# Performance work log

Measured on AMD Instinct MI355X. Metric: run time of the kernel, lower is better.

## Reference

```python
import jax, jax.numpy as jnp
import numpy as np

K_GAUSS = 7      # gaussian_kernel_size
K_CONV = 5       # base-kernel conv size
SIGMA_MIN = 0.01
SIGMA_MAX = 1.0


def setup_inputs() -> dict:
    key = jax.random.key(0)
    k1, k2, k3 = jax.random.split(key, 3)
    input_data = jax.random.normal(k1, (8, 3, 224, 224), dtype=jnp.float32)
    foa_xy = jax.random.randint(k2, (8, 2), 0, 224)  # (x=row, y=col) fixation per sample
    weight = jax.random.normal(k3, (64, 3, K_CONV, K_CONV), dtype=jnp.float32) * 0.05
    return {"input_data": input_data, "foa_xy": foa_xy, "weight": weight}


def _extract_patches(x, k):
    # torch.nn.functional.unfold with stride=1, dilation=1, padding=k//2
    # x: (b,c,h,w) -> (b,c,k*k,h*w); patch flat index = ki*k + kj (row-major)
    b, c, h, w = x.shape
    p = k // 2
    xp = jnp.pad(x, ((0, 0), (0, 0), (p, p), (p, p)))
    shifts = [xp[:, :, i:i + h, j:j + w] for i in range(k) for j in range(k)]
    return jnp.stack(shifts, axis=2).reshape(b, c, k * k, h * w)


def _gaussian_modulate(x, foa_xy):
    # GaussianFOAConv2d: per-pixel normalized Gaussian kernel, sigma linear in distance from FOA
    b, c, h, w = x.shape
    hw = h * w
    ii, jj = jnp.meshgrid(jnp.arange(h, dtype=jnp.float32),
                          jnp.arange(w, dtype=jnp.float32), indexing='ij')
    xy = jnp.stack([ii, jj], axis=-1).reshape(hw, 2)           # (hw,2): (row, col)
    foa = foa_xy.astype(jnp.float32)                            # (b,2)
    dists = jnp.linalg.norm(xy[None, :, :] - foa[:, None, :], axis=-1)
    dists = dists / np.float32(np.sqrt(h ** 2 + w ** 2))        # (b,hw) in [0,1]
    sigmas = (1.0 - dists) * SIGMA_MIN + dists * SIGMA_MAX      # (b,hw)
    r = jnp.arange(-(K_GAUSS // 2), K_GAUSS // 2 + 1, dtype=jnp.float32)
    d2 = (r[:, None] ** 2 + r[None, :] ** 2).reshape(-1)        # (kk,) row-major, matches patch order
    kern = jnp.exp(-d2[None, :, None] / (2.0 * sigmas[:, None, :] ** 2))  # (b,kk,hw)
    kern = kern / jnp.sum(kern, axis=1, keepdims=True)
    patches = _extract_patches(x, K_GAUSS)                      # (b,c,kk,hw)
    out = jnp.einsum('bckp,bkp->bcp', patches, kern)            # spatial-only kernel -> sum over kk
    return out.reshape(b, c, h, w)


def reference(input_data, foa_xy, weight):
    # 1) Gaussian input modulation driven by FOA distance
    modulated = _gaussian_modulate(input_data, foa_xy)
    # 2) classic convolution with the learnable base kernel (stride 1, 'same' padding, no bias)
    p = K_CONV // 2
    return jax.lax.conv_general_dilated(
        modulated, weight, window_strides=(1, 1), padding=((p, p), (p, p)),
        dimension_numbers=('NCHW', 'OIHW', 'NCHW'))
```

## Files before the change

### kernel.cpp

```cpp
#include <hip/hip_runtime.h>

#define H 224
#define W 224
#define HW (224 * 224)
#define CIN 3
#define OCH 64

#define TS 32
#define MN 36
#define MSTH 40
#define RN 42
#define RST 44

typedef __attribute__((ext_vector_type(8))) short short8;
typedef __attribute__((ext_vector_type(4))) float f32x4;

__device__ __forceinline__ unsigned f2bf_pk(float lo, float hi) {
    unsigned a = __float_as_uint(lo), b = __float_as_uint(hi);
    a = (a + 0x7FFFu + ((a >> 16) & 1u)) >> 16;
    b = (b + 0x7FFFu + ((b >> 16) & 1u)) & 0xFFFF0000u;
    return a | b;
}

__global__ void make_wA(const float* __restrict__ w, uint4* __restrict__ wA) {
    int t = threadIdx.x;
    int lane = t & 63;
    int fi = t >> 6;
    int mt = fi >> 2, S = fi & 3;
    int q = lane >> 4;
    int oc = mt * 16 + (lane & 15);
    float v[8];
#pragma unroll
    for (int j = 0; j < 8; ++j) {
        float x = 0.f;
        if (j < 5) {
            if (S < 3) x = w[oc * 75 + S * 25 + q * 5 + j];
            else if (q < 3) x = w[oc * 75 + q * 25 + 20 + j];
        }
        v[j] = x;
    }
    uint4 r;
    r.x = f2bf_pk(v[0], v[1]);
    r.y = f2bf_pk(v[2], v[3]);
    r.z = f2bf_pk(v[4], v[5]);
    r.w = f2bf_pk(v[6], v[7]);
    wA[fi * 64 + lane] = r;
}

__global__ __launch_bounds__(256, 2) void fused(
    const uint4* __restrict__ wA, const float* __restrict__ in,
    const int* __restrict__ foa, float* __restrict__ out)
{
    __shared__ float  s_raw[CIN][RN][RST];
    __shared__ ushort s_mod[CIN][MN][MSTH];

    int tid = threadIdx.x;
    int lane = tid & 63;
    int tx0 = blockIdx.x * TS, ty0 = blockIdx.y * TS, b = blockIdx.z;

    short8 aw[4][4];
#pragma unroll
    for (int mt = 0; mt < 4; ++mt)
#pragma unroll
        for (int S = 0; S < 4; ++S) {
            union { uint4 u4; short8 s8; } cv;
            cv.u4 = wA[(mt * 4 + S) * 64 + lane];
            aw[mt][S] = cv.s8;
        }

    const float* src = in + (size_t)b * CIN * HW;
    for (int i = tid; i < CIN * RN * RN; i += 256) {
        int ch = i / (RN * RN);
        int rem = i - ch * (RN * RN);
        int rr = rem / RN;
        int cc = rem - rr * RN;
        int gr = ty0 - 5 + rr, gc = tx0 - 5 + cc;
        float v = 0.f;
        if ((unsigned)gr < H && (unsigned)gc < W) v = src[ch * HW + gr * W + gc];
        s_raw[ch][rr][cc] = v;
    }
    __syncthreads();

    float fr = (float)foa[2 * b + 0], fc = (float)foa[2 * b + 1];
    for (int u = tid; u < CIN * MN * 9; u += 256) {
        int ch = u / (MN * 9);
        int rem = u - ch * (MN * 9);
        int rm = rem / 9;
        int qc = rem - rm * 9;
        int cm0 = qc * 4;
        int gr = ty0 - 2 + rm;

        float pw[4][7], inv[4];
#pragma unroll
        for (int o = 0; o < 4; ++o) {
            int gc = tx0 - 2 + cm0 + o;
            float dr = (float)gr - fr, dc = (float)gc - fc;
            float dist = sqrtf(dr * dr + dc * dc) * 3.1567268e-3f;
            float sigma = 0.01f + 0.99f * dist;
            float ae = -0.5f / (sigma * sigma);
            float e1 = __expf(ae);
            float e2 = e1 * e1, e4 = e2 * e2, e9 = e4 * e4 * e1;
            pw[o][0] = e9; pw[o][1] = e4; pw[o][2] = e1; pw[o][3] = 1.f;
            pw[o][4] = e1; pw[o][5] = e4; pw[o][6] = e9;
            float S = 1.f + 2.f * (e1 + e4 + e9);
            inv[o] = 1.f / (S * S);
        }
        float acc[4] = {0.f, 0.f, 0.f, 0.f};
#pragma unroll
        for (int ki = 0; ki < 7; ++ki) {
            const float* rp = &s_raw[ch][rm + ki][cm0];
            float rv[10];
            *(f32x4*)&rv[0] = *(const f32x4*)rp;
            *(f32x4*)&rv[4] = *(const f32x4*)(rp + 4);
            *(float2*)&rv[8] = *(const float2*)(rp + 8);
#pragma unroll
            for (int o = 0; o < 4; ++o) {
                float rs = 0.f;
#pragma unroll
                for (int kj = 0; kj < 7; ++kj) rs += pw[o][kj] * rv[o + kj];
                acc[o] += pw[o][ki] * rs;
            }
        }
        float res[4];
#pragma unroll
        for (int o = 0; o < 4; ++o) {
            int gc = tx0 - 2 + cm0 + o;
            bool ok = ((unsigned)gr < H) && ((unsigned)gc < W);
            res[o] = ok ? acc[o] * inv[o] : 0.f;
        }
        uint2 st;
        st.x = f2bf_pk(res[0], res[1]);
        st.y = f2bf_pk(res[2], res[3]);
        *(uint2*)&s_mod[ch][rm][cm0] = st;
    }
    __syncthreads();

    int wv = tid >> 6;
    int q = lane >> 4, li = lane & 15;

#pragma unroll
    for (int r8 = 0; r8 < 8; ++r8) {
        int ro = wv * 8 + r8;
#pragma unroll
        for (int s = 0; s < 2; ++s) {
            int co = s * 16 + li;
            int cd = co >> 1;
            unsigned sel = (unsigned)(co & 1) * 16u;

            short8 bf[4];
#pragma unroll
            for (int S = 0; S < 4; ++S) {
                int ch = (S < 3) ? S : (q < 3 ? q : 2);
                int rm = (S < 3) ? (ro + q) : (ro + 4);
                const unsigned* p = (const unsigned*)&s_mod[ch][rm][0] + cd;
                unsigned u0 = p[0], u1 = p[1], u2 = p[2];
                union { unsigned u[4]; short8 s8; } cv;
                cv.u[0] = __builtin_amdgcn_alignbit(u1, u0, sel);
                cv.u[1] = __builtin_amdgcn_alignbit(u2, u1, sel);
                cv.u[2] = u2 >> sel;
                cv.u[3] = 0;
                bf[S] = cv.s8;
            }

            f32x4 acc[4];
#pragma unroll
            for (int mt = 0; mt < 4; ++mt) acc[mt] = (f32x4){0.f, 0.f, 0.f, 0.f};
#pragma unroll
            for (int S = 0; S < 4; ++S)
#pragma unroll
                for (int mt = 0; mt < 4; ++mt)
                    acc[mt] = __builtin_amdgcn_mfma_f32_16x16x32_bf16(
                        aw[mt][S], bf[S], acc[mt], 0, 0, 0);

            int px = tx0 + co, py = ty0 + ro;
#pragma unroll
            for (int mt = 0; mt < 4; ++mt) {
#pragma unroll
                for (int r = 0; r < 4; ++r) {
                    int oc = mt * 16 + q * 4 + r;
                    out[(size_t)(b * OCH + oc) * HW + (size_t)py * W + px] = acc[mt][r];
                }
            }
        }
    }
}

extern "C" void kernel_launch(void* const* d_in, const int* in_sizes, int n_in,
                              void* d_out, int out_size, void* d_ws, size_t ws_size,
                              hipStream_t stream) {
    const float* input  = (const float*)d_in[0];
    const int*   foa    = (const int*)d_in[1];
    const float* weight = (const float*)d_in[2];
    float* outp = (float*)d_out;

    uint4* wA = (uint4*)d_ws;

    make_wA<<<1, 1024, 0, stream>>>(weight, wA);

    dim3 grid(W / TS, H / TS, 8);
    fused<<<grid, 256, 0, stream>>>(wA, input, foa, outp);
}
```

Baseline: 126.4 us.

## Give each wave a private halo tile to remove block-wide barriers

Each of the four waves now loads its own 18x42 raw halo and computes its own 12-row modulated strip in a private shared-memory slice, so the two __syncthreads are dropped and waves proceed independently. The goal is to remove barrier stalls and let each wave's load, Gaussian and MFMA phases overlap with those of other waves. In exchange, halo rows are loaded and modulated redundantly across waves (18 rows per 8 output rows instead of 42 per 32), and shared memory grows to about 51 KB, which may limit occupancy. No barrier is needed within a wave because the writes and reads stay inside a single wavefront.

```diff
diff --git a/kernel.cpp b/kernel.cpp
--- a/kernel.cpp
+++ b/kernel.cpp
@@ -7,10 +7,12 @@
 #define OCH 64
 
 #define TS 32
-#define MN 36
-#define MSTH 40
-#define RN 42
-#define RST 44
+#define WRN 18
+#define WRC 42
+#define WRST 44
+#define WMN 12
+#define WMC 36
+#define WMST 40
 
 typedef __attribute__((ext_vector_type(8))) short short8;
 typedef __attribute__((ext_vector_type(4))) float f32x4;
@@ -51,12 +53,15 @@
     const uint4* __restrict__ wA, const float* __restrict__ in,
     const int* __restrict__ foa, float* __restrict__ out)
 {
-    __shared__ float  s_raw[CIN][RN][RST];
-    __shared__ ushort s_mod[CIN][MN][MSTH];
+    __shared__ float  s_raw[4][CIN][WRN][WRST];
+    __shared__ ushort s_mod[4][CIN][WMN][WMST];
 
     int tid = threadIdx.x;
     int lane = tid & 63;
-    int tx0 = blockIdx.x * TS, ty0 = blockIdx.y * TS, b = blockIdx.z;
+    int wv = tid >> 6;
+    int tx0 = blockIdx.x * TS;
+    int ty0 = blockIdx.y * TS + wv * 8;
+    int b = blockIdx.z;
 
     short8 aw[4][4];
 #pragma unroll
@@ -69,22 +74,21 @@
         }
 
     const float* src = in + (size_t)b * CIN * HW;
-    for (int i = tid; i < CIN * RN * RN; i += 256) {
-        int ch = i / (RN * RN);
-        int rem = i - ch * (RN * RN);
-        int rr = rem / RN;
-        int cc = rem - rr * RN;
+    for (int i = lane; i < CIN * WRN * WRC; i += 64) {
+        int ch = i / (WRN * WRC);
+        int rem = i - ch * (WRN * WRC);
+        int rr = rem / WRC;
+        int cc = rem - rr * WRC;
         int gr = ty0 - 5 + rr, gc = tx0 - 5 + cc;
         float v = 0.f;
         if ((unsigned)gr < H && (unsigned)gc < W) v = src[ch * HW + gr * W + gc];
-        s_raw[ch][rr][cc] = v;
-    }
-    __syncthreads();
+        s_raw[wv][ch][rr][cc] = v;
+    }
 
     float fr = (float)foa[2 * b + 0], fc = (float)foa[2 * b + 1];
-    for (int u = tid; u < CIN * MN * 9; u += 256) {
-        int ch = u / (MN * 9);
-        int rem = u - ch * (MN * 9);
+    for (int u = lane; u < CIN * WMN * 9; u += 64) {
+        int ch = u / (WMN * 9);
+        int rem = u - ch * (WMN * 9);
         int rm = rem / 9;
         int qc = rem - rm * 9;
         int cm0 = qc * 4;
@@ -108,7 +112,7 @@
         float acc[4] = {0.f, 0.f, 0.f, 0.f};
 #pragma unroll
         for (int ki = 0; ki < 7; ++ki) {
-            const float* rp = &s_raw[ch][rm + ki][cm0];
+            const float* rp = &s_raw[wv][ch][rm + ki][cm0];
             float rv[10];
             *(f32x4*)&rv[0] = *(const f32x4*)rp;
             *(f32x4*)&rv[4] = *(const f32x4*)(rp + 4);
@@ -131,16 +135,13 @@
         uint2 st;
         st.x = f2bf_pk(res[0], res[1]);
         st.y = f2bf_pk(res[2], res[3]);
-        *(uint2*)&s_mod[ch][rm][cm0] = st;
-    }
-    __syncthreads();
-
-    int wv = tid >> 6;
+        *(uint2*)&s_mod[wv][ch][rm][cm0] = st;
+    }
+
     int q = lane >> 4, li = lane & 15;
 
 #pragma unroll
     for (int r8 = 0; r8 < 8; ++r8) {
-        int ro = wv * 8 + r8;
 #pragma unroll
         for (int s = 0; s < 2; ++s) {
             int co = s * 16 + li;
@@ -151,8 +152,8 @@
 #pragma unroll
             for (int S = 0; S < 4; ++S) {
                 int ch = (S < 3) ? S : (q < 3 ? q : 2);
-                int rm = (S < 3) ? (ro + q) : (ro + 4);
-                const unsigned* p = (const unsigned*)&s_mod[ch][rm][0] + cd;
+                int rm = (S < 3) ? (r8 + q) : (r8 + 4);
+                const unsigned* p = (const unsigned*)&s_mod[wv][ch][rm][0] + cd;
                 unsigned u0 = p[0], u1 = p[1], u2 = p[2];
                 union { unsigned u[4]; short8 s8; } cv;
                 cv.u[0] = __builtin_amdgcn_alignbit(u1, u0, sel);
@@ -172,7 +173,7 @@
                     acc[mt] = __builtin_amdgcn_mfma_f32_16x16x32_bf16(
                         aw[mt][S], bf[S], acc[mt], 0, 0, 0);
 
-            int px = tx0 + co, py = ty0 + ro;
+            int px = tx0 + co, py = ty0 + r8;
 #pragma unroll
             for (int mt = 0; mt < 4; ++mt) {
 #pragma unroll
```

Result: slower. 135.8 us (+7.5%).

## Fold weight packing into fused kernel and use nontemporal output stores

Applied to the files above, without the earlier changes.

Removes the separate make_wA kernel launch. Each block now copies the 64x75 fp32 weights into shared memory and packs its own bf16 MFMA A-fragments. Output stores become nontemporal to avoid polluting cache with the large write-once result. The cost is 19.2KB of extra LDS per block, which may reduce occupancy, and redundant weight conversion in every block.

```diff
diff --git a/kernel.cpp b/kernel.cpp
--- a/kernel.cpp
+++ b/kernel.cpp
@@ -22,51 +22,17 @@
     return a | b;
 }
 
-__global__ void make_wA(const float* __restrict__ w, uint4* __restrict__ wA) {
-    int t = threadIdx.x;
-    int lane = t & 63;
-    int fi = t >> 6;
-    int mt = fi >> 2, S = fi & 3;
-    int q = lane >> 4;
-    int oc = mt * 16 + (lane & 15);
-    float v[8];
-#pragma unroll
-    for (int j = 0; j < 8; ++j) {
-        float x = 0.f;
-        if (j < 5) {
-            if (S < 3) x = w[oc * 75 + S * 25 + q * 5 + j];
-            else if (q < 3) x = w[oc * 75 + q * 25 + 20 + j];
-        }
-        v[j] = x;
-    }
-    uint4 r;
-    r.x = f2bf_pk(v[0], v[1]);
-    r.y = f2bf_pk(v[2], v[3]);
-    r.z = f2bf_pk(v[4], v[5]);
-    r.w = f2bf_pk(v[6], v[7]);
-    wA[fi * 64 + lane] = r;
-}
-
 __global__ __launch_bounds__(256, 2) void fused(
-    const uint4* __restrict__ wA, const float* __restrict__ in,
-    const int* __restrict__ foa, float* __restrict__ out)
+    const float* __restrict__ in, const int* __restrict__ foa,
+    const float* __restrict__ w, float* __restrict__ out)
 {
     __shared__ float  s_raw[CIN][RN][RST];
     __shared__ ushort s_mod[CIN][MN][MSTH];
+    __shared__ float  s_w[OCH * CIN * 25];
 
     int tid = threadIdx.x;
     int lane = tid & 63;
     int tx0 = blockIdx.x * TS, ty0 = blockIdx.y * TS, b = blockIdx.z;
-
-    short8 aw[4][4];
-#pragma unroll
-    for (int mt = 0; mt < 4; ++mt)
-#pragma unroll
-        for (int S = 0; S < 4; ++S) {
-            union { uint4 u4; short8 s8; } cv;
-            cv.u4 = wA[(mt * 4 + S) * 64 + lane];
-            aw[mt][S] = cv.s8;
-        }
 
     const float* src = in + (size_t)b * CIN * HW;
     for (int i = tid; i < CIN * RN * RN; i += 256) {
@@ -79,7 +45,36 @@
         if ((unsigned)gr < H && (unsigned)gc < W) v = src[ch * HW + gr * W + gc];
         s_raw[ch][rr][cc] = v;
     }
+    for (int i = tid; i < 1200; i += 256)
+        *(f32x4*)&s_w[i * 4] = *(const f32x4*)&w[i * 4];
     __syncthreads();
+
+    int wv = tid >> 6;
+    int q = lane >> 4, li = lane & 15;
+    short8 aw[4][4];
+#pragma unroll
+    for (int mt = 0; mt < 4; ++mt) {
+        int oc = mt * 16 + li;
+#pragma unroll
+        for (int S = 0; S < 4; ++S) {
+            float v[8];
+#pragma unroll
+            for (int j = 0; j < 8; ++j) {
+                float x = 0.f;
+                if (j < 5) {
+                    if (S < 3)      x = s_w[oc * 75 + S * 25 + q * 5 + j];
+                    else if (q < 3) x = s_w[oc * 75 + q * 25 + 20 + j];
+                }
+                v[j] = x;
+            }
+            union { unsigned u[4]; short8 s8; } cv;
+            cv.u[0] = f2bf_pk(v[0], v[1]);
+            cv.u[1] = f2bf_pk(v[2], v[3]);
+            cv.u[2] = f2bf_pk(v[4], v[5]);
+            cv.u[3] = f2bf_pk(v[6], v[7]);
+            aw[mt][S] = cv.s8;
+        }
+    }
 
     float fr = (float)foa[2 * b + 0], fc = (float)foa[2 * b + 1];
     for (int u = tid; u < CIN * MN * 9; u += 256) {
@@ -135,9 +130,6 @@
     }
     __syncthreads();
 
-    int wv = tid >> 6;
-    int q = lane >> 4, li = lane & 15;
-
 #pragma unroll
     for (int r8 = 0; r8 < 8; ++r8) {
         int ro = wv * 8 + r8;
@@ -178,7 +170,9 @@
 #pragma unroll
                 for (int r = 0; r < 4; ++r) {
                     int oc = mt * 16 + q * 4 + r;
-                    out[(size_t)(b * OCH + oc) * HW + (size_t)py * W + px] = acc[mt][r];
+                    __builtin_nontemporal_store(
+                        acc[mt][r],
+                        &out[(size_t)(b * OCH + oc) * HW + (size_t)py * W + px]);
                 }
             }
         }
@@ -193,10 +187,6 @@
     const float* weight = (const float*)d_in[2];
     float* outp = (float*)d_out;
 
-    uint4* wA = (uint4*)d_ws;
-
-    make_wA<<<1, 1024, 0, stream>>>(weight, wA);
-
     dim3 grid(W / TS, H / TS, 8);
-    fused<<<grid, 256, 0, stream>>>(wA, input, foa, outp);
+    fused<<<grid, 256, 0, stream>>>(input, foa, weight, outp);
 }
```

Result: slower. 142.4 us (+12.7%).
